# Optimization experiments

Hardware: AMD Instinct MI355X
Metric: run time of the kernel (lower is better)

Reference implementation:

```python
import jax, jax.numpy as jnp
import numpy as np

B, N, DIM, HEADS = 8, 512, 512, 16
MAX_DIST, NG = 128, 32
RBF_STOP = 20.0
EPS = 1e-5


def _ln(x, g, b):
    m = jnp.mean(x, axis=-1, keepdims=True)
    v = jnp.mean((x - m) ** 2, axis=-1, keepdims=True)
    return (x - m) * jax.lax.rsqrt(v + EPS) * g + b


def setup_inputs() -> dict:
    key = jax.random.key(0)
    ks = jax.random.split(key, 12)
    d = DIM
    s = 0.02
    return {
        "x": jax.random.normal(ks[0], (B * N, d), jnp.float32),
        "dist_matrix": jax.random.randint(ks[1], (B, N, N), 0, MAX_DIST, jnp.int32),
        "dist_3d": jax.random.uniform(ks[2], (B, N, N), jnp.float32) * RBF_STOP,
        "norm1_g": jnp.ones((d,), jnp.float32),
        "norm1_b": jnp.zeros((d,), jnp.float32),
        "in_proj_w": jax.random.normal(ks[3], (3 * d, d), jnp.float32) * s,
        "in_proj_b": jnp.zeros((3 * d,), jnp.float32),
        "out_proj_w": jax.random.normal(ks[4], (d, d), jnp.float32) * s,
        "out_proj_b": jnp.zeros((d,), jnp.float32),
        "dist_emb": jax.random.normal(ks[5], (MAX_DIST, HEADS), jnp.float32) * s,
        "rbf_w": jax.random.normal(ks[6], (HEADS, NG), jnp.float32) * s,
        "rbf_b": jnp.zeros((HEADS,), jnp.float32),
        "norm2_g": jnp.ones((d,), jnp.float32),
        "norm2_b": jnp.zeros((d,), jnp.float32),
        "ffn_w1": jax.random.normal(ks[7], (4 * d, d), jnp.float32) * s,
        "ffn_b1": jnp.zeros((4 * d,), jnp.float32),
        "ffn_w2": jax.random.normal(ks[8], (d, 4 * d), jnp.float32) * s,
        "ffn_b2": jnp.zeros((d,), jnp.float32),
        "batch": jnp.repeat(jnp.arange(B, dtype=jnp.int32), N),
    }


def reference(x, dist_matrix, dist_3d, norm1_g, norm1_b, in_proj_w, in_proj_b,
              out_proj_w, out_proj_b, dist_emb, rbf_w, rbf_b, norm2_g, norm2_b,
              ffn_w1, ffn_b1, ffn_w2, ffn_b2, batch):
    b, n = dist_matrix.shape[0], dist_matrix.shape[1]
    d = x.shape[-1]
    dh = d // HEADS
    # equal-size graphs -> to_dense_batch is a reshape, mask all-true
    xd = x.reshape(b, n, d)

    # additive attention bias: shortest-path-distance embedding + RBF projection
    dc = jnp.clip(dist_matrix, 0, MAX_DIST - 1)
    bias_spd = dist_emb[dc]                                  # [b, n, n, H]
    offset = jnp.linspace(0.0, RBF_STOP, NG, dtype=jnp.float32)
    coeff = -0.5 / (RBF_STOP / (NG - 1)) ** 2
    rbf = jnp.exp(coeff * (dist_3d[..., None] - offset) ** 2)  # [b, n, n, NG]
    bias_3d = rbf @ rbf_w.T + rbf_b                          # [b, n, n, H]
    bias = jnp.transpose(bias_spd + bias_3d, (0, 3, 1, 2))   # [b, H, n, n]

    # multi-head attention (pre-norm residual, as in source)
    h = _ln(xd, norm1_g, norm1_b)
    qkv = h @ in_proj_w.T + in_proj_b
    q, k, v = jnp.split(qkv, 3, axis=-1)
    q = q.reshape(b, n, HEADS, dh).transpose(0, 2, 1, 3)
    k = k.reshape(b, n, HEADS, dh).transpose(0, 2, 1, 3)
    v = v.reshape(b, n, HEADS, dh).transpose(0, 2, 1, 3)
    scores = jnp.einsum('bhqd,bhkd->bhqk', q, k) / jnp.sqrt(jnp.float32(dh)) + bias
    attn = jax.nn.softmax(scores, axis=-1)
    ctx = jnp.einsum('bhqk,bhkd->bhqd', attn, v)
    ctx = ctx.transpose(0, 2, 1, 3).reshape(b, n, d)
    attn_out = ctx @ out_proj_w.T + out_proj_b
    h = h + attn_out

    # FFN (dropout inactive at eval)
    h2 = _ln(h, norm2_g, norm2_b)
    ff = jax.nn.gelu(h2 @ ffn_w1.T + ffn_b1, approximate=False) @ ffn_w2.T + ffn_b2
    h = h + ff
    return h.reshape(b * n, d)
```

## Files before the change

kernel.cpp:

```cpp
#include <hip/hip_runtime.h>
#include <hip/hip_bf16.h>
#include <math.h>

#define BB 8
#define NN 512
#define DD 512
#define NH 16
#define DH 32
#define TD 1536
#define NG 32
#define MAXD 128

typedef __attribute__((ext_vector_type(8))) short bf16x8;
typedef __attribute__((ext_vector_type(4))) float f32x4;

__device__ inline short f2bf(float x) {
    __hip_bfloat16 h = __float2bfloat16(x);
    return *reinterpret_cast<short*>(&h);
}
__device__ inline float bf2f(short x) {
    union { unsigned u; float f; } c;
    c.u = ((unsigned)(unsigned short)x) << 16;
    return c.f;
}

__device__ inline void gld_lds16(const void* g, void* l) {
    __builtin_amdgcn_global_load_lds(
        (const __attribute__((address_space(1))) unsigned int*)g,
        (__attribute__((address_space(3))) unsigned int*)l, 16, 0, 0);
}

__global__ __launch_bounds__(256) void cvt_weights(
    const float* __restrict__ s0, const float* __restrict__ s1,
    const float* __restrict__ s2, const float* __restrict__ s3,
    short* __restrict__ d0, short* __restrict__ d1,
    short* __restrict__ d2, short* __restrict__ d3,
    int n0, int n1, int n2, int n3) {
    const float* s; short* d; int n;
    switch (blockIdx.y) {
        case 0: s = s0; d = d0; n = n0; break;
        case 1: s = s1; d = d1; n = n1; break;
        case 2: s = s2; d = d2; n = n2; break;
        default: s = s3; d = d3; n = n3; break;
    }
    const int i = (blockIdx.x * 256 + threadIdx.x) * 4;
    if (i >= n) return;
    const float4 v = *(const float4*)(s + i);
    short4 o;
    o.x = f2bf(v.x); o.y = f2bf(v.y); o.z = f2bf(v.z); o.w = f2bf(v.w);
    *(short4*)(d + i) = o;
}

__global__ __launch_bounds__(256) void ln_kernel(const float* __restrict__ x,
                                                 const float* __restrict__ g,
                                                 const float* __restrict__ b,
                                                 short* __restrict__ out_bf,
                                                 float* __restrict__ out_f) {
    const int row = blockIdx.x;
    const int tid = threadIdx.x;
    const float* xr = x + (size_t)row * DD;
    float v0 = xr[tid], v1 = xr[tid + 256];
    __shared__ float s1[256], s2[256];
    s1[tid] = v0 + v1;
    s2[tid] = v0 * v0 + v1 * v1;
    __syncthreads();
    for (int off = 128; off > 0; off >>= 1) {
        if (tid < off) { s1[tid] += s1[tid + off]; s2[tid] += s2[tid + off]; }
        __syncthreads();
    }
    const float mean = s1[0] * (1.0f / DD);
    const float var  = s2[0] * (1.0f / DD) - mean * mean;
    const float rs   = rsqrtf(var + 1e-5f);
    const float o0 = (v0 - mean) * rs * g[tid] + b[tid];
    const float o1 = (v1 - mean) * rs * g[tid + 256] + b[tid + 256];
    out_bf[(size_t)row * DD + tid]       = f2bf(o0);
    out_bf[(size_t)row * DD + tid + 256] = f2bf(o1);
    if (out_f) {
        out_f[(size_t)row * DD + tid]       = o0;
        out_f[(size_t)row * DD + tid + 256] = o1;
    }
}

template <int TM, bool GELU, bool RES, int OUT>
__global__ __launch_bounds__(256) void gemm_bf16(
    const short* __restrict__ A, const short* __restrict__ Bw,
    const float* __restrict__ bias, const float* __restrict__ res,
    void* __restrict__ Cout, int M, int Nout, int K) {
    const int MI = TM / 32;
    const int bm = blockIdx.y * TM;
    const int bn = blockIdx.x * 128;
    const int tid  = threadIdx.x;
    const int wave = tid >> 6;
    const int lane = tid & 63;
    const int l16  = lane & 15;
    const int quad = lane >> 4;
    const int wr = (wave >> 1) * (TM / 2);
    const int wc = (wave & 1) * 64;

    __shared__ short As[TM * 32];
    __shared__ short Bs[128 * 32];

    f32x4 acc[MI][4];
#pragma unroll
    for (int i = 0; i < MI; i++)
#pragma unroll
        for (int j = 0; j < 4; j++) acc[i][j] = (f32x4){0.f, 0.f, 0.f, 0.f};

    for (int k0 = 0; k0 < K; k0 += 32) {
        const short* Ab = A + (size_t)bm * K + k0;
        const short* Bb = Bw + (size_t)bn * K + k0;
#pragma unroll
        for (int j = 0; j < TM / 64; j++) {
            const int idx = j * 256 + wave * 64 + lane;
            gld_lds16(Ab + (size_t)(idx >> 2) * K + (idx & 3) * 8,
                      (short*)As + (size_t)(j * 256 + wave * 64) * 8);
        }
#pragma unroll
        for (int j = 0; j < 2; j++) {
            const int idx = j * 256 + wave * 64 + lane;
            gld_lds16(Bb + (size_t)(idx >> 2) * K + (idx & 3) * 8,
                      (short*)Bs + (size_t)(j * 256 + wave * 64) * 8);
        }
        __syncthreads();
        bf16x8 af[MI], bfr[4];
#pragma unroll
        for (int i = 0; i < MI; i++)
            af[i] = *(const bf16x8*)&As[(wr + i * 16 + l16) * 32 + quad * 8];
#pragma unroll
        for (int j = 0; j < 4; j++)
            bfr[j] = *(const bf16x8*)&Bs[(wc + j * 16 + l16) * 32 + quad * 8];
#pragma unroll
        for (int i = 0; i < MI; i++)
#pragma unroll
            for (int j = 0; j < 4; j++)
                acc[i][j] = __builtin_amdgcn_mfma_f32_16x16x32_bf16(af[i], bfr[j], acc[i][j], 0, 0, 0);
        __syncthreads();
    }
#pragma unroll
    for (int i = 0; i < MI; i++) {
#pragma unroll
        for (int r = 0; r < 4; r++) {
            const int row = bm + wr + i * 16 + quad * 4 + r;
#pragma unroll
            for (int j = 0; j < 4; j++) {
                const int col = bn + wc + j * 16 + l16;
                float v = acc[i][j][r] + bias[col];
                if (GELU) v = 0.5f * v * (1.0f + erff(v * 0.70710678118654752f));
                if (RES)  v += res[(size_t)row * Nout + col];
                if (OUT == 1) ((short*)Cout)[(size_t)row * Nout + col] = f2bf(v);
                else          ((float*)Cout)[(size_t)row * Nout + col] = v;
            }
        }
    }
}

__global__ __launch_bounds__(512) void attn_mfma(
    const short* __restrict__ qkv,
    const int* __restrict__ dist,
    const float* __restrict__ dist3d,
    const float* __restrict__ demb,
    const float* __restrict__ rbfw,
    const float* __restrict__ rbfb,
    float* __restrict__ O_part,
    float* __restrict__ l_part)
{
    const int blk  = blockIdx.x;
    const int b    = blk & 7;
    const int part = (blk >> 3) & 3;
    const int q0   = (blk >> 5) * 16;
    const int tid  = threadIdx.x;
    const int wave = tid >> 6;
    const int lane = tid & 63;
    const int l16  = lane & 15;
    const int quad = lane >> 4;

    __shared__ short Kc[NH * 16 * 32];
    __shared__ short Vc[NH * 16 * 32];
    __shared__ short biasB[16 * 16 * 24];
    __shared__ short Pb[8 * 16 * 32];

    for (int i = tid; i < 8 * 16 * 32; i += 512) Pb[i] = 0;

    const float scale = 0.17677669529663687f;
    bf16x8 qf[2];
#pragma unroll
    for (int h = 0; h < 2; h++) {
        const int hh = wave * 2 + h;
        qf[h] = *(const bf16x8*)(qkv + (size_t)(b * NN + q0 + l16) * TD + hh * DH + quad * 8);
    }
    bf16x8 wf;
#pragma unroll
    for (int j = 0; j < 8; j++) wf[j] = f2bf(rbfw[l16 * NG + quad * 8 + j]);

    f32x4 O[2][2];
    float lsum[2][4];
#pragma unroll
    for (int h = 0; h < 2; h++) {
#pragma unroll
        for (int t = 0; t < 2; t++) O[h][t] = (f32x4){0.f, 0.f, 0.f, 0.f};
#pragma unroll
        for (int r = 0; r < 4; r++) lsum[h][r] = 0.f;
    }

    const float STEP  = 20.0f / 31.0f;
    const float COEFF = -0.5f / (STEP * STEP);

    for (int c = 0; c < 8; c++) {
        const int k0 = part * 128 + c * 16;
        __syncthreads();
#pragma unroll
        for (int l = 0; l < 4; l++) {
            const int idxb = l * 512 + wave * 64;
            const int idx  = idxb + lane;
            const int kk2  = idx & 1023;
            const int h = kk2 >> 6, k = (kk2 >> 2) & 15, c4 = kk2 & 3;
            const short* src = qkv + (size_t)(b * NN + k0 + k) * TD +
                               DD * (1 + (l >> 1)) + h * 32 + c4 * 8;
            short* dstb = (l < 2 ? (short*)Kc : (short*)Vc) + (size_t)(idxb & 1023) * 8;
            gld_lds16(src, dstb);
        }
#pragma unroll
        for (int g = 0; g < 2; g++) {
            const int qloc = wave * 2 + g;
            const size_t rowbase = ((size_t)(b * NN) + q0 + qloc) * NN + k0;
            const float d3 = dist3d[rowbase + l16];
            bf16x8 ef;
#pragma unroll
            for (int j = 0; j < 8; j++) {
                const float t = d3 - (float)(quad * 8 + j) * STEP;
                ef[j] = f2bf(__expf(COEFF * t * t));
            }
            f32x4 cc;
            const float rb = rbfb[l16];
#pragma unroll
            for (int r = 0; r < 4; r++) {
                int dc = dist[rowbase + quad * 4 + r];
                dc = min(max(dc, 0), MAXD - 1);
                cc[r] = demb[dc * NH + l16] + rb;
            }
            const f32x4 dres = __builtin_amdgcn_mfma_f32_16x16x32_bf16(ef, wf, cc, 0, 0, 0);
#pragma unroll
            for (int r = 0; r < 4; r++)
                biasB[(qloc * 16 + quad * 4 + r) * 24 + l16] = f2bf(dres[r]);
        }
        __syncthreads();
#pragma unroll
        for (int h = 0; h < 2; h++) {
            const int hh = wave * 2 + h;
            const bf16x8 kf = *(const bf16x8*)&Kc[hh * 512 + l16 * 32 + quad * 8];
            f32x4 s = __builtin_amdgcn_mfma_f32_16x16x32_bf16(
                qf[h], kf, (f32x4){0.f, 0.f, 0.f, 0.f}, 0, 0, 0);
            float pv[4];
#pragma unroll
            for (int r = 0; r < 4; r++) {
                float sv = s[r] * scale + bf2f(biasB[((quad * 4 + r) * 16 + l16) * 24 + hh]);
                sv = fminf(sv, 20.f);
                pv[r] = __expf(sv);
                lsum[h][r] += pv[r];
                Pb[wave * 512 + (quad * 4 + r) * 32 + l16] = f2bf(pv[r]);
            }
            const bf16x8 pf = *(const bf16x8*)&Pb[wave * 512 + l16 * 32 + quad * 8];
#pragma unroll
            for (int t = 0; t < 2; t++) {
                bf16x8 vf;
                if (quad < 2) {
#pragma unroll
                    for (int j = 0; j < 8; j++)
                        vf[j] = Vc[hh * 512 + (quad * 8 + j) * 32 + t * 16 + l16];
                } else {
#pragma unroll
                    for (int j = 0; j < 8; j++) vf[j] = 0;
                }
                O[h][t] = __builtin_amdgcn_mfma_f32_16x16x32_bf16(pf, vf, O[h][t], 0, 0, 0);
            }
        }
    }
    const size_t poff = (size_t)part * 4096;
#pragma unroll
    for (int h = 0; h < 2; h++) {
        const int hh = wave * 2 + h;
#pragma unroll
        for (int m = 1; m < 16; m <<= 1)
#pragma unroll
            for (int r = 0; r < 4; r++) lsum[h][r] += __shfl_xor(lsum[h][r], m);
#pragma unroll
        for (int r = 0; r < 4; r++) {
            const size_t row = (size_t)(b * NN + q0 + quad * 4 + r);
#pragma unroll
            for (int t = 0; t < 2; t++)
                O_part[(poff + row) * DD + hh * DH + t * 16 + l16] = O[h][t][r];
            if (l16 == 0) l_part[(poff + row) * NH + hh] = lsum[h][r];
        }
    }
}

__global__ __launch_bounds__(256) void attn_combine(
    const float* __restrict__ O_part, const float* __restrict__ l_part,
    short* __restrict__ ctx) {
    const int e = (blockIdx.x * 256 + threadIdx.x) * 4;
    const int row = e >> 9, d = e & 511, h = d >> 5;
    const size_t PO = (size_t)4096 * 512;
    const float4 o0 = *(const float4*)(O_part + e);
    const float4 o1 = *(const float4*)(O_part + PO + e);
    const float4 o2 = *(const float4*)(O_part + 2 * PO + e);
    const float4 o3 = *(const float4*)(O_part + 3 * PO + e);
    const int li = row * NH + h;
    const float l = l_part[li] + l_part[4096 * NH + li] +
                    l_part[2 * 4096 * NH + li] + l_part[3 * 4096 * NH + li];
    const float rinv = 1.0f / l;
    short4 o;
    o.x = f2bf((o0.x + o1.x + o2.x + o3.x) * rinv);
    o.y = f2bf((o0.y + o1.y + o2.y + o3.y) * rinv);
    o.z = f2bf((o0.z + o1.z + o2.z + o3.z) * rinv);
    o.w = f2bf((o0.w + o1.w + o2.w + o3.w) * rinv);
    *(short4*)(ctx + e) = o;
}

extern "C" void kernel_launch(void* const* d_in, const int* in_sizes, int n_in,
                              void* d_out, int out_size, void* d_ws, size_t ws_size,
                              hipStream_t stream) {
    const float* x      = (const float*)d_in[0];
    const int*   dist   = (const int*)d_in[1];
    const float* dist3d = (const float*)d_in[2];
    const float* n1g    = (const float*)d_in[3];
    const float* n1b    = (const float*)d_in[4];
    const float* win    = (const float*)d_in[5];
    const float* bin    = (const float*)d_in[6];
    const float* wo     = (const float*)d_in[7];
    const float* bo     = (const float*)d_in[8];
    const float* demb   = (const float*)d_in[9];
    const float* rbfw   = (const float*)d_in[10];
    const float* rbfb   = (const float*)d_in[11];
    const float* n2g    = (const float*)d_in[12];
    const float* n2b    = (const float*)d_in[13];
    const float* w1     = (const float*)d_in[14];
    const float* b1     = (const float*)d_in[15];
    const float* w2     = (const float*)d_in[16];
    const float* b2     = (const float*)d_in[17];

    char* p = (char*)d_ws;
    short* h_bf   = (short*)p; p += (size_t)4096 * 512 * 2;
    float* h_f    = (float*)p; p += (size_t)4096 * 512 * 4;
    short* qkv_bf = (short*)p; p += (size_t)4096 * 1536 * 2;
    short* ctx_bf = (short*)p; p += (size_t)4096 * 512 * 2;
    float* hres   = (float*)p; p += (size_t)4096 * 512 * 4;
    short* h2_bf  = (short*)p; p += (size_t)4096 * 512 * 2;
    short* win_bf = (short*)p; p += (size_t)1536 * 512 * 2;
    short* wo_bf  = (short*)p; p += (size_t)512 * 512 * 2;
    short* w1_bf  = (short*)p; p += (size_t)2048 * 512 * 2;
    short* w2_bf  = (short*)p; p += (size_t)512 * 2048 * 2;
    float* O_part = (float*)p;
    short* mid_bf = (short*)p;
    p += (size_t)4 * 4096 * 512 * 4;
    float* l_part = (float*)p; p += (size_t)4 * 4096 * 16 * 4;

    const int M = BB * NN;

    cvt_weights<<<dim3(1024, 4), 256, 0, stream>>>(
        win, wo, w1, w2, win_bf, wo_bf, w1_bf, w2_bf,
        1536 * 512, 512 * 512, 2048 * 512, 512 * 2048);
    ln_kernel<<<M, 256, 0, stream>>>(x, n1g, n1b, h_bf, h_f);
    gemm_bf16<128, false, false, 1><<<dim3(12, 32), 256, 0, stream>>>(
        h_bf, win_bf, bin, nullptr, qkv_bf, M, TD, DD);
    attn_mfma<<<1024, 512, 0, stream>>>(
        qkv_bf, dist, dist3d, demb, rbfw, rbfb, O_part, l_part);
    attn_combine<<<2048, 256, 0, stream>>>(O_part, l_part, ctx_bf);
    gemm_bf16<64, false, true, 0><<<dim3(4, 64), 256, 0, stream>>>(
        ctx_bf, wo_bf, bo, h_f, hres, M, DD, DD);
    ln_kernel<<<M, 256, 0, stream>>>(hres, n2g, n2b, h2_bf, nullptr);
    gemm_bf16<128, true, false, 1><<<dim3(16, 32), 256, 0, stream>>>(
        h2_bf, w1_bf, b1, nullptr, mid_bf, M, 2048, DD);
    gemm_bf16<64, false, true, 0><<<dim3(4, 64), 256, 0, stream>>>(
        mid_bf, w2_bf, b2, hres, (float*)d_out, M, DD, 2048);
}
```

Measured before the change: 277.3 us.

## Replace per-element RBF bias computation with interpolated lookup table; split keys into three

A small kernel precomputes the RBF-projected bias per head at 130 points over [0,20]. The attention kernel now builds the bias from linear interpolation in that table plus a bf16 shared-memory copy of the distance embedding, held in registers. This drops the per-element exps, the bias MFMA and the biasB shared buffer. The key range is also split into three parts instead of four (768 blocks), which shrinks the partial buffers and the combine work. The cost is interpolation and bf16 approximation error in the bias, redundant dist and dist3d loads across waves, and fewer blocks for parallelism.

```diff
diff --git a/kernel.cpp b/kernel.cpp
--- a/kernel.cpp
+++ b/kernel.cpp
@@ -49,6 +49,24 @@
     short4 o;
     o.x = f2bf(v.x); o.y = f2bf(v.y); o.z = f2bf(v.z); o.w = f2bf(v.w);
     *(short4*)(d + i) = o;
+}
+
+__global__ __launch_bounds__(256) void rbf_table(
+    const float* __restrict__ rbfw, const float* __restrict__ rbfb,
+    short* __restrict__ Tg) {
+    const int idx = blockIdx.x * 256 + threadIdx.x;
+    if (idx >= 130 * 16) return;
+    const int i = idx >> 4, h = idx & 15;
+    const float STEP  = 20.0f / 31.0f;
+    const float COEFF = -0.5f / (STEP * STEP);
+    const float x = fminf((float)i, 128.0f) * (20.0f / 128.0f);
+    float acc = rbfb[h];
+#pragma unroll
+    for (int g = 0; g < NG; g++) {
+        const float t = x - (float)g * STEP;
+        acc += __expf(COEFF * t * t) * rbfw[h * NG + g];
+    }
+    Tg[idx] = f2bf(acc);
 }
 
 __global__ __launch_bounds__(256) void ln_kernel(const float* __restrict__ x,
@@ -159,15 +177,15 @@
     const int* __restrict__ dist,
     const float* __restrict__ dist3d,
     const float* __restrict__ demb,
-    const float* __restrict__ rbfw,
-    const float* __restrict__ rbfb,
+    const short* __restrict__ Tg,
     float* __restrict__ O_part,
     float* __restrict__ l_part)
 {
     const int blk  = blockIdx.x;
     const int b    = blk & 7;
-    const int part = (blk >> 3) & 3;
-    const int q0   = (blk >> 5) * 16;
+    const int t3   = blk >> 3;
+    const int part = t3 % 3;
+    const int q0   = (t3 / 3) * 16;
     const int tid  = threadIdx.x;
     const int wave = tid >> 6;
     const int lane = tid & 63;
@@ -176,10 +194,13 @@
 
     __shared__ short Kc[NH * 16 * 32];
     __shared__ short Vc[NH * 16 * 32];
-    __shared__ short biasB[16 * 16 * 24];
     __shared__ short Pb[8 * 16 * 32];
+    __shared__ short Tt[130 * 18];
+    __shared__ short Db[128 * 18];
 
     for (int i = tid; i < 8 * 16 * 32; i += 512) Pb[i] = 0;
+    for (int i = tid; i < 130 * 16; i += 512) Tt[(i >> 4) * 18 + (i & 15)] = Tg[i];
+    for (int i = tid; i < 128 * 16; i += 512) Db[(i >> 4) * 18 + (i & 15)] = f2bf(demb[i]);
 
     const float scale = 0.17677669529663687f;
     bf16x8 qf[2];
@@ -188,25 +209,22 @@
         const int hh = wave * 2 + h;
         qf[h] = *(const bf16x8*)(qkv + (size_t)(b * NN + q0 + l16) * TD + hh * DH + quad * 8);
     }
-    bf16x8 wf;
-#pragma unroll
-    for (int j = 0; j < 8; j++) wf[j] = f2bf(rbfw[l16 * NG + quad * 8 + j]);
 
     f32x4 O[2][2];
     float lsum[2][4];
 #pragma unroll
     for (int h = 0; h < 2; h++) {
 #pragma unroll
-        for (int t = 0; t < 2; t++) O[h][t] = (f32x4){0.f, 0.f, 0.f, 0.f};
+        for (int tt = 0; tt < 2; tt++) O[h][tt] = (f32x4){0.f, 0.f, 0.f, 0.f};
 #pragma unroll
         for (int r = 0; r < 4; r++) lsum[h][r] = 0.f;
     }
 
-    const float STEP  = 20.0f / 31.0f;
-    const float COEFF = -0.5f / (STEP * STEP);
-
-    for (int c = 0; c < 8; c++) {
-        const int k0 = part * 128 + c * 16;
+    const int cbeg = part * 11;
+    const int cend = (part == 2) ? 32 : cbeg + 11;
+
+    for (int c = cbeg; c < cend; c++) {
+        const int k0 = c * 16;
         __syncthreads();
 #pragma unroll
         for (int l = 0; l < 4; l++) {
@@ -219,29 +237,22 @@
             short* dstb = (l < 2 ? (short*)Kc : (short*)Vc) + (size_t)(idxb & 1023) * 8;
             gld_lds16(src, dstb);
         }
-#pragma unroll
-        for (int g = 0; g < 2; g++) {
-            const int qloc = wave * 2 + g;
-            const size_t rowbase = ((size_t)(b * NN) + q0 + qloc) * NN + k0;
-            const float d3 = dist3d[rowbase + l16];
-            bf16x8 ef;
-#pragma unroll
-            for (int j = 0; j < 8; j++) {
-                const float t = d3 - (float)(quad * 8 + j) * STEP;
-                ef[j] = f2bf(__expf(COEFF * t * t));
+        float biasr[2][4];
+        {
+            const int hh0 = wave * 2, hh1 = hh0 + 1;
+#pragma unroll
+            for (int r = 0; r < 4; r++) {
+                const size_t off = ((size_t)(b * NN) + q0 + quad * 4 + r) * NN + k0 + l16;
+                int dc = dist[off];
+                dc = min(max(dc, 0), MAXD - 1);
+                const float x = dist3d[off] * 6.4f;
+                int ii = (int)x; ii = min(ii, 127);
+                const float fr = x - (float)ii;
+                const float t00 = bf2f(Tt[ii * 18 + hh0]), t01 = bf2f(Tt[ii * 18 + 18 + hh0]);
+                const float t10 = bf2f(Tt[ii * 18 + hh1]), t11 = bf2f(Tt[ii * 18 + 18 + hh1]);
+                biasr[0][r] = bf2f(Db[dc * 18 + hh0]) + t00 + (t01 - t00) * fr;
+                biasr[1][r] = bf2f(Db[dc * 18 + hh1]) + t10 + (t11 - t10) * fr;
             }
-            f32x4 cc;
-            const float rb = rbfb[l16];
-#pragma unroll
-            for (int r = 0; r < 4; r++) {
-                int dc = dist[rowbase + quad * 4 + r];
-                dc = min(max(dc, 0), MAXD - 1);
-                cc[r] = demb[dc * NH + l16] + rb;
-            }
-            const f32x4 dres = __builtin_amdgcn_mfma_f32_16x16x32_bf16(ef, wf, cc, 0, 0, 0);
-#pragma unroll
-            for (int r = 0; r < 4; r++)
-                biasB[(qloc * 16 + quad * 4 + r) * 24 + l16] = f2bf(dres[r]);
         }
         __syncthreads();
 #pragma unroll
@@ -253,7 +264,7 @@
             float pv[4];
 #pragma unroll
             for (int r = 0; r < 4; r++) {
-                float sv = s[r] * scale + bf2f(biasB[((quad * 4 + r) * 16 + l16) * 24 + hh]);
+                float sv = s[r] * scale + biasr[h][r];
                 sv = fminf(sv, 20.f);
                 pv[r] = __expf(sv);
                 lsum[h][r] += pv[r];
@@ -261,17 +272,17 @@
             }
             const bf16x8 pf = *(const bf16x8*)&Pb[wave * 512 + l16 * 32 + quad * 8];
 #pragma unroll
-            for (int t = 0; t < 2; t++) {
+            for (int tt = 0; tt < 2; tt++) {
                 bf16x8 vf;
                 if (quad < 2) {
 #pragma unroll
                     for (int j = 0; j < 8; j++)
-                        vf[j] = Vc[hh * 512 + (quad * 8 + j) * 32 + t * 16 + l16];
+                        vf[j] = Vc[hh * 512 + (quad * 8 + j) * 32 + tt * 16 + l16];
                 } else {
 #pragma unroll
                     for (int j = 0; j < 8; j++) vf[j] = 0;
                 }
-                O[h][t] = __builtin_amdgcn_mfma_f32_16x16x32_bf16(pf, vf, O[h][t], 0, 0, 0);
+                O[h][tt] = __builtin_amdgcn_mfma_f32_16x16x32_bf16(pf, vf, O[h][tt], 0, 0, 0);
             }
         }
     }
@@ -287,8 +298,8 @@
         for (int r = 0; r < 4; r++) {
             const size_t row = (size_t)(b * NN + q0 + quad * 4 + r);
 #pragma unroll
-            for (int t = 0; t < 2; t++)
-                O_part[(poff + row) * DD + hh * DH + t * 16 + l16] = O[h][t][r];
+            for (int tt = 0; tt < 2; tt++)
+                O_part[(poff + row) * DD + hh * DH + tt * 16 + l16] = O[h][tt][r];
             if (l16 == 0) l_part[(poff + row) * NH + hh] = lsum[h][r];
         }
     }
@@ -303,16 +314,14 @@
     const float4 o0 = *(const float4*)(O_part + e);
     const float4 o1 = *(const float4*)(O_part + PO + e);
     const float4 o2 = *(const float4*)(O_part + 2 * PO + e);
-    const float4 o3 = *(const float4*)(O_part + 3 * PO + e);
     const int li = row * NH + h;
-    const float l = l_part[li] + l_part[4096 * NH + li] +
-                    l_part[2 * 4096 * NH + li] + l_part[3 * 4096 * NH + li];
+    const float l = l_part[li] + l_part[4096 * NH + li] + l_part[2 * 4096 * NH + li];
     const float rinv = 1.0f / l;
     short4 o;
-    o.x = f2bf((o0.x + o1.x + o2.x + o3.x) * rinv);
-    o.y = f2bf((o0.y + o1.y + o2.y + o3.y) * rinv);
-    o.z = f2bf((o0.z + o1.z + o2.z + o3.z) * rinv);
-    o.w = f2bf((o0.w + o1.w + o2.w + o3.w) * rinv);
+    o.x = f2bf((o0.x + o1.x + o2.x) * rinv);
+    o.y = f2bf((o0.y + o1.y + o2.y) * rinv);
+    o.z = f2bf((o0.z + o1.z + o2.z) * rinv);
+    o.w = f2bf((o0.w + o1.w + o2.w) * rinv);
     *(short4*)(ctx + e) = o;
 }
 
@@ -349,21 +358,23 @@
     short* wo_bf  = (short*)p; p += (size_t)512 * 512 * 2;
     short* w1_bf  = (short*)p; p += (size_t)2048 * 512 * 2;
     short* w2_bf  = (short*)p; p += (size_t)512 * 2048 * 2;
+    short* Tg     = (short*)p; p += (size_t)8192;
     float* O_part = (float*)p;
     short* mid_bf = (short*)p;
-    p += (size_t)4 * 4096 * 512 * 4;
-    float* l_part = (float*)p; p += (size_t)4 * 4096 * 16 * 4;
+    p += (size_t)3 * 4096 * 512 * 4;
+    float* l_part = (float*)p; p += (size_t)3 * 4096 * 16 * 4;
 
     const int M = BB * NN;
 
     cvt_weights<<<dim3(1024, 4), 256, 0, stream>>>(
         win, wo, w1, w2, win_bf, wo_bf, w1_bf, w2_bf,
         1536 * 512, 512 * 512, 2048 * 512, 512 * 2048);
+    rbf_table<<<9, 256, 0, stream>>>(rbfw, rbfb, Tg);
     ln_kernel<<<M, 256, 0, stream>>>(x, n1g, n1b, h_bf, h_f);
     gemm_bf16<128, false, false, 1><<<dim3(12, 32), 256, 0, stream>>>(
         h_bf, win_bf, bin, nullptr, qkv_bf, M, TD, DD);
-    attn_mfma<<<1024, 512, 0, stream>>>(
-        qkv_bf, dist, dist3d, demb, rbfw, rbfb, O_part, l_part);
+    attn_mfma<<<768, 512, 0, stream>>>(
+        qkv_bf, dist, dist3d, demb, Tg, O_part, l_part);
     attn_combine<<<2048, 256, 0, stream>>>(O_part, l_part, ctx_bf);
     gemm_bf16<64, false, true, 0><<<dim3(4, 64), 256, 0, stream>>>(
         ctx_bf, wo_bf, bo, h_f, hres, M, DD, DD);
```

Measured after the change: 267.2 us. 3.6% less time.
